# Optimization experiments

Hardware: AMD Instinct MI355X
Metric: run time of the kernel (lower is better)

The kernel has to match this reference:

```python
import jax, jax.numpy as jnp
import numpy as np

N = 20000          # num proposals (nodes)
E = 320000         # num edges
IN = 4096          # roi feature dim
EMB = 200          # glove embed dim
HID = 512          # hidden dim
NH = 8             # heads (conv1)
HC = HID // NH     # 64 per-head channels
NCLS = 151         # VG object classes
NEG_SLOPE = 0.2    # PyG GATConv leaky_relu slope


def setup_inputs() -> dict:
    key = jax.random.key(0)
    ks = jax.random.split(key, 18)
    d_in1 = IN + EMB + 128  # 4424, conv1 input dim
    inp = {
        "roi_features": jax.random.normal(ks[0], (N, IN), jnp.float32),
        "box_info": jax.random.uniform(ks[1], (N, 9), jnp.float32),
        # embedding tables
        "emb1": jax.random.normal(ks[2], (NCLS, EMB), jnp.float32) * 0.02,
        "emb2": jax.random.normal(ks[3], (NCLS, EMB), jnp.float32) * 0.02,
        # bbox MLP 9 -> 32 -> 128
        "bw1": jax.random.normal(ks[4], (9, 32), jnp.float32) / np.sqrt(9),
        "bb1": jnp.zeros((32,), jnp.float32),
        "bw2": jax.random.normal(ks[5], (32, 128), jnp.float32) / np.sqrt(32),
        "bb2": jnp.zeros((128,), jnp.float32),
        # GATConv1: d_in1 -> 8 heads x 64, concat
        "W1": jax.random.normal(ks[6], (d_in1, NH * HC), jnp.float32) / np.sqrt(d_in1),
        "a_src1": jax.random.normal(ks[7], (NH, HC), jnp.float32) * 0.1,
        "a_dst1": jax.random.normal(ks[8], (NH, HC), jnp.float32) * 0.1,
        "bias1": jnp.zeros((NH * HC,), jnp.float32),
        # GATConv2: 512 -> 512, 1 head, concat=False
        "W2": jax.random.normal(ks[9], (HID, HID), jnp.float32) / np.sqrt(HID),
        "a_src2": jax.random.normal(ks[10], (1, HID), jnp.float32) * 0.1,
        "a_dst2": jax.random.normal(ks[11], (1, HID), jnp.float32) * 0.1,
        "bias2": jnp.zeros((HID,), jnp.float32),
        # int inputs
        "obj_labels": jax.random.randint(ks[12], (N,), 0, NCLS, jnp.int32),
        "edge_index": jax.random.randint(ks[13], (2, E), 0, N, jnp.int32),
    }
    return inp


def _segment_softmax(logits, seg, n):
    # logits: [E, H]; softmax over edges sharing the same destination seg id
    m = jax.ops.segment_max(logits, seg, num_segments=n)
    e = jnp.exp(logits - m[seg])
    s = jax.ops.segment_sum(e, seg, num_segments=n)
    return e / (s[seg] + 1e-16)


def _gat_conv(x, src, dst, W, a_src, a_dst, bias, concat):
    # PyG GATConv (self-loops already included in src/dst); dropout off (eval)
    n = x.shape[0]
    H, C = a_src.shape
    h = (x @ W).reshape(n, H, C)                      # [N, H, C]
    al_s = jnp.einsum('nhc,hc->nh', h, a_src)         # [N, H]
    al_d = jnp.einsum('nhc,hc->nh', h, a_dst)
    logits = jax.nn.leaky_relu(al_s[src] + al_d[dst], NEG_SLOPE)  # [E, H]
    alpha = _segment_softmax(logits, dst, n)          # [E, H]
    out = jax.ops.segment_sum(alpha[:, :, None] * h[src], dst, num_segments=n)
    out = out.reshape(n, H * C) if concat else out.mean(axis=1)
    return out + bias


def reference(roi_features, box_info, emb1, emb2, bw1, bb1, bw2, bb2,
              W1, a_src1, a_dst1, bias1, W2, a_src2, a_dst2, bias2,
              obj_labels, edge_index):
    n = roi_features.shape[0]
    # predcls mode: GT labels -> embedding lookup
    obj_embed = emb1[obj_labels]                              # [N, 200]
    pos = jax.nn.relu(box_info @ bw1 + bb1)
    pos = jax.nn.relu(pos @ bw2 + bb2)                        # [N, 128]
    x = jnp.concatenate([roi_features, obj_embed, pos], -1)  # [N, 4424]

    # add self-loops (PyG GATConv default)
    ar = jnp.arange(n, dtype=edge_index.dtype)
    src = jnp.concatenate([edge_index[0], ar])
    dst = jnp.concatenate([edge_index[1], ar])

    edge_f1 = jax.nn.elu(_gat_conv(x, src, dst, W1, a_src1, a_dst1, bias1, True))
    obj_feats = _gat_conv(edge_f1, src, dst, W2, a_src2, a_dst2, bias2, False)

    obj_dists = jax.nn.one_hot(obj_labels, NCLS, dtype=jnp.float32)
    edge_pre_rep = jnp.concatenate([roi_features, obj_feats, emb2[obj_labels]], -1)
    return obj_dists, obj_labels, edge_pre_rep
```

## Files before the change

### kernel.cpp

```cpp
#include <hip/hip_runtime.h>
#include <hip/hip_bf16.h>

#define NNODES 20000
#define NEDGES 320000
#define ETOT   (NEDGES + NNODES)
#define KPADX  4224
#define SK     4
#define KC     (KPADX / SK)
#define MPAD   20096
#define NCLS   151
#define EPRW   4808
#define OUT_LAB_OFF  3020000L
#define OUT_EPR_OFF  3040000L
#define NSLOPE 0.2f

typedef __attribute__((ext_vector_type(8))) short bf16x8;
typedef __attribute__((ext_vector_type(4))) float f32x4;
typedef __attribute__((ext_vector_type(4))) short s16x4;

__device__ __forceinline__ short f2bf(float v) {
  union { __hip_bfloat16 b; short s; } u;
  u.b = __float2bfloat16(v);
  return u.s;
}

__device__ __forceinline__ float bf2f(short s) {
  union { float f; unsigned u; } x;
  x.u = ((unsigned)(unsigned short)s) << 16;
  return x.f;
}

__device__ __forceinline__ void gld16(const short* g, short* l) {
  __builtin_amdgcn_global_load_lds(
      (const __attribute__((address_space(1))) unsigned int*)g,
      (__attribute__((address_space(3))) unsigned int*)l, 16, 0, 0);
}

#define QB0 10000
#define QB1 (QB0 + 5000)
#define QB2 (QB1 + 1584)
#define QB3 (QB2 + 2112)
#define QB4 (QB3 + 256)
#define QB5 (QB4 + 1329)
#define QB6 (QB5 + 151)

__global__ __launch_bounds__(256) void mega_prep_kernel(
    const float* __restrict__ roi, const float* __restrict__ box,
    const float* __restrict__ emb1, const float* __restrict__ emb2,
    const float* __restrict__ bw1, const float* __restrict__ bb1,
    const float* __restrict__ bw2, const float* __restrict__ bb2,
    const float* __restrict__ W1, const float* __restrict__ W2,
    const int* __restrict__ labels, const int* __restrict__ ei,
    short* __restrict__ x, short* __restrict__ w1t, short* __restrict__ w2t,
    short* __restrict__ ef1, int* __restrict__ deg,
    float* __restrict__ als2, float* __restrict__ ald2,
    float* __restrict__ E1, float* __restrict__ dout) {
  const int b = blockIdx.x;
  const int tid = threadIdx.x;

  __shared__ float hids[4][32];
  __shared__ float tile[32][33];

  if (b < QB0) {
    const int base = b * 2048 + tid;
    f32x4 v[8];
#pragma unroll
    for (int k = 0; k < 8; ++k)
      v[k] = *(const f32x4*)&roi[(long)(base + k * 256) * 4];
#pragma unroll
    for (int k = 0; k < 8; ++k) {
      const int t = base + k * 256;
      const int node = t >> 10, cq = t & 1023;
      __builtin_nontemporal_store(v[k],
          (f32x4*)&dout[OUT_EPR_OFF + (long)node * EPRW + cq * 4]);
      s16x4 bb;
      bb.x = f2bf(v[k].x); bb.y = f2bf(v[k].y);
      bb.z = f2bf(v[k].z); bb.w = f2bf(v[k].w);
      *(s16x4*)&x[(long)node * KPADX + cq * 4] = bb;
    }
  } else if (b < QB1) {
    const int w = tid >> 6;
    const int lane = tid & 63;
    const int nd = (b - QB0) * 4 + w;
    if (lane < 32) {
      float a = bb1[lane];
#pragma unroll
      for (int i = 0; i < 9; ++i) a += box[nd * 9 + i] * bw1[i * 32 + lane];
      hids[w][lane] = a > 0.f ? a : 0.f;
    }
    __syncthreads();
    const long xrow = (long)nd * KPADX;
#pragma unroll
    for (int jj = 0; jj < 2; ++jj) {
      const int j = lane + jj * 64;
      float a = bb2[j];
#pragma unroll
      for (int i = 0; i < 32; ++i) a += hids[w][i] * bw2[i * 128 + j];
      a = a > 0.f ? a : 0.f;
      x[xrow + 4096 + j] = f2bf(a);
    }
    const int lab = labels[nd];
    float* epr = dout + OUT_EPR_OFF + (long)nd * EPRW;
    if (lane < 50) {
      const f32x4 e2 = *(const f32x4*)&emb2[lab * 200 + lane * 4];
      __builtin_nontemporal_store(e2, (f32x4*)&epr[4608 + lane * 4]);
    }
    for (int j = lane; j < NCLS; j += 64)
      dout[(long)nd * NCLS + j] = (j == lab) ? 1.f : 0.f;
    if (lane == 0) dout[OUT_LAB_OFF + nd] = (float)lab;
  } else if (b < QB2) {
    const int t = (b - QB1) * 256 + tid;
    if (t < 96 * KPADX) x[(long)NNODES * KPADX + t] = 0;
    if (t < 96 * 512)   ef1[(long)NNODES * 512 + t] = 0;
    if (t < MPAD)       { als2[t] = 0.f; ald2[t] = 0.f; }
  } else if (b < QB3) {
    const int t = b - QB2;
    const int n0 = (t % 16) * 32;
    const int k0 = (t / 16) * 32;
    const int tx = tid & 31, ty = tid >> 5;
#pragma unroll
    for (int i = ty; i < 32; i += 8) {
      const int kp = k0 + i;
      const int src = kp < 4096 ? kp : kp + 200;
      tile[i][tx] = W1[(long)src * 512 + (n0 + tx)];
    }
    __syncthreads();
#pragma unroll
    for (int i = ty; i < 32; i += 8)
      w1t[(long)(n0 + i) * KPADX + (k0 + tx)] = f2bf(tile[tx][i]);
  } else if (b < QB4) {
    const int t = b - QB3;
    const int n0 = (t % 16) * 32;
    const int k0 = (t / 16) * 32;
    const int tx = tid & 31, ty = tid >> 5;
#pragma unroll
    for (int i = ty; i < 32; i += 8)
      tile[i][tx] = W2[(long)(k0 + i) * 512 + (n0 + tx)];
    __syncthreads();
#pragma unroll
    for (int i = ty; i < 32; i += 8)
      w2t[(long)(n0 + i) * 512 + (k0 + tx)] = f2bf(tile[tx][i]);
  } else if (b < QB5) {
    const int e = (b - QB4) * 256 + tid;
    if (e < ETOT) {
      const int d = (e < NEDGES) ? ei[NEDGES + e] : (e - NEDGES);
      atomicAdd(&deg[d], 1);
    }
  } else {
    const int c = b - QB5;
#pragma unroll
    for (int jj = 0; jj < 2; ++jj) {
      const int j = tid + jj * 256;
      float a = 0.f;
      for (int k = 0; k < 200; ++k)
        a += emb1[c * 200 + k] * W1[(long)(4096 + k) * 512 + j];
      E1[c * 512 + j] = a;
    }
  }
}

__global__ __launch_bounds__(256) void scan_kernel(const int* __restrict__ deg,
                                                   int* __restrict__ off,
                                                   int* __restrict__ cur) {
  __shared__ int part[256];
  const int tid = threadIdx.x;
  const int chunk = (NNODES + 255) / 256;
  int start = tid * chunk;
  int end = start + chunk; if (end > NNODES) end = NNODES;
  int s = 0;
  for (int i = start; i < end; ++i) s += deg[i];
  part[tid] = s;
  __syncthreads();
  for (int d = 1; d < 256; d <<= 1) {
    const int v = (tid >= d) ? part[tid - d] : 0;
    __syncthreads();
    part[tid] += v;
    __syncthreads();
  }
  int base = part[tid] - s;
  for (int i = start; i < end; ++i) { off[i] = base; cur[i] = base; base += deg[i]; }
}

__global__ void csr_fill_kernel(const int* __restrict__ ei, int* __restrict__ cur,
                                int* __restrict__ csrs) {
  const int e = blockIdx.x * 256 + threadIdx.x;
  if (e >= ETOT) return;
  const int s = (e < NEDGES) ? ei[e] : (e - NEDGES);
  const int d = (e < NEDGES) ? ei[NEDGES + e] : (e - NEDGES);
  unsigned slot = (unsigned)atomicAdd(&cur[d], 1);
  if (slot >= ETOT) slot = 0;
  csrs[slot] = s;
}

__global__ __launch_bounds__(256) void gemm_split(const short* __restrict__ A,
                                                  const short* __restrict__ BT,
                                                  short* __restrict__ hp) {
  __shared__ short As[2][4096];
  __shared__ short Bs[2][4096];
  const int tid = threadIdx.x;
  const int lane = tid & 63;
  const int w = tid >> 6;
  const int wr = w >> 1, wc = w & 1;
  const int wid = (blockIdx.x & 7) * 314 + ((int)blockIdx.x >> 3);
  const long bm = (long)(wid >> 4) * 128;
  const int  sk = (wid >> 2) & 3;
  const long bn = (long)(wid & 3) * 128;

  f32x4 acc[4][4] = {};

  const int ksw = ((lane & 3) ^ ((lane >> 3) & 3)) * 8;
  const short* gA0 = A + (bm + w * 32 + (lane >> 2)) * (long)KPADX + sk * KC + ksw;
  const short* gA1 = gA0 + 16L * KPADX;
  const short* gB0 = BT + (bn + w * 32 + (lane >> 2)) * (long)KPADX + sk * KC + ksw;
  const short* gB1 = gB0 + 16L * KPADX;

  const int lofs = w * 1024;
  const int sw = ((lane >> 4) ^ (((lane & 15) >> 1) & 3)) * 8;
  const int ar = (wr * 64 + (lane & 15)) * 32 + sw;
  const int br = (wc * 64 + (lane & 15)) * 32 + sw;

  gld16(gA0, &As[0][lofs]); gld16(gA1, &As[0][lofs + 512]);
  gld16(gB0, &Bs[0][lofs]); gld16(gB1, &Bs[0][lofs + 512]);
  gA0 += 32; gA1 += 32; gB0 += 32; gB1 += 32;

  const int NT = KC / 32;
  int cur = 0;
  for (int t = 0; t < NT; ++t) {
    if (t + 1 < NT) {
      gld16(gA0, &As[cur ^ 1][lofs]); gld16(gA1, &As[cur ^ 1][lofs + 512]);
      gld16(gB0, &Bs[cur ^ 1][lofs]); gld16(gB1, &Bs[cur ^ 1][lofs + 512]);
      gA0 += 32; gA1 += 32; gB0 += 32; gB1 += 32;
      asm volatile("s_waitcnt vmcnt(4)" ::: "memory");
    } else {
      asm volatile("s_waitcnt vmcnt(0)" ::: "memory");
    }
    __builtin_amdgcn_s_barrier();
    bf16x8 a[4], b[4];
#pragma unroll
    for (int mi = 0; mi < 4; ++mi) a[mi] = *(const bf16x8*)&As[cur][ar + mi * 512];
#pragma unroll
    for (int ni = 0; ni < 4; ++ni) b[ni] = *(const bf16x8*)&Bs[cur][br + ni * 512];
#pragma unroll
    for (int mi = 0; mi < 4; ++mi)
#pragma unroll
      for (int ni = 0; ni < 4; ++ni)
        acc[mi][ni] = __builtin_amdgcn_mfma_f32_16x16x32_bf16(a[mi], b[ni], acc[mi][ni], 0, 0, 0);
    __builtin_amdgcn_s_barrier();
    cur ^= 1;
  }

  short* Cp = hp + (long)sk * MPAD * 512;
#pragma unroll
  for (int mi = 0; mi < 4; ++mi) {
#pragma unroll
    for (int ni = 0; ni < 4; ++ni) {
      const long row0 = bm + wr * 64 + mi * 16 + (lane >> 4) * 4;
      const long col  = bn + wc * 64 + ni * 16 + (lane & 15);
#pragma unroll
      for (int r = 0; r < 4; ++r)
        Cp[(row0 + r) * 512 + col] = f2bf(acc[mi][ni][r]);
    }
  }
}

__global__ __launch_bounds__(256) void reduce1_kernel(short* __restrict__ hp,
    const float* __restrict__ E1, const int* __restrict__ labels,
    const float* __restrict__ aS, const float* __restrict__ aD,
    float* __restrict__ als, float* __restrict__ ald) {
  const int row = blockIdx.x * 4 + (threadIdx.x >> 6);
  const int lane = threadIdx.x & 63;
  const int c0 = lane * 8;
  const long base = (long)row * 512 + c0;
  float v[8] = {};
#pragma unroll
  for (int s = 0; s < SK; ++s) {
    const bf16x8 p = *(const bf16x8*)&hp[(long)s * MPAD * 512 + base];
#pragma unroll
    for (int j = 0; j < 8; ++j) v[j] += bf2f(p[j]);
  }
  const int lab = (row < NNODES) ? labels[row] : 0;
  const float* e1r = E1 + (long)lab * 512;
#pragma unroll
  for (int j = 0; j < 8; ++j) v[j] += e1r[c0 + j];
  bf16x8 o;
#pragma unroll
  for (int j = 0; j < 8; ++j) o[j] = f2bf(v[j]);
  *(bf16x8*)&hp[base] = o;
  float s_ = 0.f, d_ = 0.f;
#pragma unroll
  for (int j = 0; j < 8; ++j) {
    s_ += v[j] * aS[c0 + j];
    d_ += v[j] * aD[c0 + j];
  }
#pragma unroll
  for (int oo = 1; oo < 8; oo <<= 1) {
    s_ += __shfl_xor(s_, oo);
    d_ += __shfl_xor(d_, oo);
  }
  if ((lane & 7) == 0) {
    const int head = lane >> 3;
    als[row * 8 + head] = s_;
    ald[row * 8 + head] = d_;
  }
}

__global__ __launch_bounds__(256) void gemm_bt(const short* __restrict__ A,
                                               const short* __restrict__ BT,
                                               short* __restrict__ C,
                                               const float* __restrict__ aS,
                                               const float* __restrict__ aD,
                                               float* __restrict__ als,
                                               float* __restrict__ ald,
                                               int Kpad, int Ncols, int H) {
  __shared__ short As[2][4096];
  __shared__ short Bs[2][4096];
  const int tid = threadIdx.x;
  const int lane = tid & 63;
  const int w = tid >> 6;
  const int wr = w >> 1, wc = w & 1;
  const int nbn = Ncols >> 7;
  const long bm = (long)((int)blockIdx.x / nbn) * 128;
  const long bn = (long)((int)blockIdx.x % nbn) * 128;

  f32x4 acc[4][4] = {};

  const int ksw = ((lane & 3) ^ ((lane >> 3) & 3)) * 8;
  const short* gA0 = A + (bm + w * 32 + (lane >> 2)) * (long)Kpad + ksw;
  const short* gA1 = gA0 + 16L * Kpad;
  const short* gB0 = BT + (bn + w * 32 + (lane >> 2)) * (long)Kpad + ksw;
  const short* gB1 = gB0 + 16L * Kpad;

  const int lofs = w * 1024;
  const int sw = ((lane >> 4) ^ (((lane & 15) >> 1) & 3)) * 8;
  const int ar = (wr * 64 + (lane & 15)) * 32 + sw;
  const int br = (wc * 64 + (lane & 15)) * 32 + sw;

  gld16(gA0, &As[0][lofs]); gld16(gA1, &As[0][lofs + 512]);
  gld16(gB0, &Bs[0][lofs]); gld16(gB1, &Bs[0][lofs + 512]);
  gA0 += 32; gA1 += 32; gB0 += 32; gB1 += 32;

  const int NT = Kpad / 32;
  int cur = 0;
  for (int t = 0; t < NT; ++t) {
    if (t + 1 < NT) {
      gld16(gA0, &As[cur ^ 1][lofs]); gld16(gA1, &As[cur ^ 1][lofs + 512]);
      gld16(gB0, &Bs[cur ^ 1][lofs]); gld16(gB1, &Bs[cur ^ 1][lofs + 512]);
      gA0 += 32; gA1 += 32; gB0 += 32; gB1 += 32;
      asm volatile("s_waitcnt vmcnt(4)" ::: "memory");
    } else {
      asm volatile("s_waitcnt vmcnt(0)" ::: "memory");
    }
    __builtin_amdgcn_s_barrier();
    bf16x8 a[4], b[4];
#pragma unroll
    for (int mi = 0; mi < 4; ++mi) a[mi] = *(const bf16x8*)&As[cur][ar + mi * 512];
#pragma unroll
    for (int ni = 0; ni < 4; ++ni) b[ni] = *(const bf16x8*)&Bs[cur][br + ni * 512];
#pragma unroll
    for (int mi = 0; mi < 4; ++mi)
#pragma unroll
      for (int ni = 0; ni < 4; ++ni)
        acc[mi][ni] = __builtin_amdgcn_mfma_f32_16x16x32_bf16(a[mi], b[ni], acc[mi][ni], 0, 0, 0);
    __builtin_amdgcn_s_barrier();
    cur ^= 1;
  }

  const int colb = (int)bn + wc * 64 + (lane & 15);

#pragma unroll
  for (int mi = 0; mi < 4; ++mi) {
#pragma unroll
    for (int ni = 0; ni < 4; ++ni) {
      const long row0 = bm + wr * 64 + mi * 16 + (lane >> 4) * 4;
      const long col  = bn + wc * 64 + ni * 16 + (lane & 15);
#pragma unroll
      for (int r = 0; r < 4; ++r)
        C[(row0 + r) * (long)Ncols + col] = f2bf(acc[mi][ni][r]);
    }
  }

  float asv[4], adv[4];
#pragma unroll
  for (int ni = 0; ni < 4; ++ni) {
    asv[ni] = aS[colb + ni * 16];
    adv[ni] = aD[colb + ni * 16];
  }
  const int head = (H == 8) ? (((int)bn >> 6) + wc) : 0;
#pragma unroll
  for (int mi = 0; mi < 4; ++mi) {
#pragma unroll
    for (int r = 0; r < 4; ++r) {
      float s = 0.f, d = 0.f;
#pragma unroll
      for (int ni = 0; ni < 4; ++ni) {
        const float v = acc[mi][ni][r];
        s += v * asv[ni];
        d += v * adv[ni];
      }
#pragma unroll
      for (int o = 1; o < 16; o <<= 1) {
        s += __shfl_xor(s, o);
        d += __shfl_xor(d, o);
      }
      if ((lane & 15) == 0) {
        const long row = bm + wr * 64 + mi * 16 + (lane >> 4) * 4 + r;
        atomicAdd(&als[row * H + head], s);
        atomicAdd(&ald[row * H + head], d);
      }
    }
  }
}

__global__ __launch_bounds__(256) void gather1_kernel(const int* __restrict__ off,
    const int* __restrict__ csrs,
    const float* __restrict__ als, const float* __restrict__ ald,
    const short* __restrict__ h1, const float* __restrict__ bias,
    short* __restrict__ ef1) {
  const int dn = blockIdx.x * 4 + (threadIdx.x >> 6);
  const int lane = threadIdx.x & 63;
  const int c0 = lane * 8;
  const int head = lane >> 3;
  const int beg = off[dn];
  const int end = (dn == NNODES - 1) ? ETOT : off[dn + 1];
  const float ad = ald[dn * 8 + head];
  float sum = 0.f;
  float acc[8] = {};
  for (int i = beg; i < end; ++i) {
    int s = csrs[i];
    if ((unsigned)s >= NNODES) s = 0;
    float l = als[s * 8 + head] + ad;
    l = l > 0.f ? l : NSLOPE * l;
    const float wgt = expf(l);
    sum += wgt;
    const bf16x8 hv = *(const bf16x8*)&h1[(long)s * 512 + c0];
#pragma unroll
    for (int j = 0; j < 8; ++j) acc[j] += wgt * bf2f(hv[j]);
  }
  const float inv = 1.f / (sum + 1e-16f);
  bf16x8 outv;
#pragma unroll
  for (int j = 0; j < 8; ++j) {
    float r = acc[j] * inv + bias[c0 + j];
    r = r > 0.f ? r : expm1f(r);
    outv[j] = f2bf(r);
  }
  *(bf16x8*)&ef1[(long)dn * 512 + c0] = outv;
}

__global__ __launch_bounds__(256) void gather2_kernel(const int* __restrict__ off,
    const int* __restrict__ csrs,
    const float* __restrict__ als, const float* __restrict__ ald,
    const short* __restrict__ h2, const float* __restrict__ bias,
    float* __restrict__ dout) {
  const int dn = blockIdx.x * 4 + (threadIdx.x >> 6);
  const int lane = threadIdx.x & 63;
  const int c0 = lane * 8;
  const int beg = off[dn];
  const int end = (dn == NNODES - 1) ? ETOT : off[dn + 1];
  const float ad = ald[dn];
  float sum = 0.f;
  float acc[8] = {};
  for (int i = beg; i < end; ++i) {
    int s = csrs[i];
    if ((unsigned)s >= NNODES) s = 0;
    float l = als[s] + ad;
    l = l > 0.f ? l : NSLOPE * l;
    const float wgt = expf(l);
    sum += wgt;
    const bf16x8 hv = *(const bf16x8*)&h2[(long)s * 512 + c0];
#pragma unroll
    for (int j = 0; j < 8; ++j) acc[j] += wgt * bf2f(hv[j]);
  }
  const float inv = 1.f / (sum + 1e-16f);
  float* epr = dout + OUT_EPR_OFF + (long)dn * EPRW + 4096;
  f32x4 o0, o1;
  o0.x = acc[0] * inv + bias[c0 + 0];
  o0.y = acc[1] * inv + bias[c0 + 1];
  o0.z = acc[2] * inv + bias[c0 + 2];
  o0.w = acc[3] * inv + bias[c0 + 3];
  o1.x = acc[4] * inv + bias[c0 + 4];
  o1.y = acc[5] * inv + bias[c0 + 5];
  o1.z = acc[6] * inv + bias[c0 + 6];
  o1.w = acc[7] * inv + bias[c0 + 7];
  __builtin_nontemporal_store(o0, (f32x4*)&epr[c0]);
  __builtin_nontemporal_store(o1, (f32x4*)&epr[c0 + 4]);
}

extern "C" void kernel_launch(void* const* d_in, const int* in_sizes, int n_in,
                              void* d_out, int out_size, void* d_ws, size_t ws_size,
                              hipStream_t stream) {
  const float* roi  = (const float*)d_in[0];
  const float* box  = (const float*)d_in[1];
  const float* emb1 = (const float*)d_in[2];
  const float* emb2 = (const float*)d_in[3];
  const float* bw1  = (const float*)d_in[4];
  const float* bb1  = (const float*)d_in[5];
  const float* bw2  = (const float*)d_in[6];
  const float* bb2  = (const float*)d_in[7];
  const float* W1   = (const float*)d_in[8];
  const float* as1  = (const float*)d_in[9];
  const float* ad1  = (const float*)d_in[10];
  const float* b1   = (const float*)d_in[11];
  const float* W2   = (const float*)d_in[12];
  const float* as2  = (const float*)d_in[13];
  const float* ad2  = (const float*)d_in[14];
  const float* b2   = (const float*)d_in[15];
  const int* labels = (const int*)d_in[16];
  const int* ei     = (const int*)d_in[17];
  float* dout = (float*)d_out;

  char* wsb = (char*)d_ws;
  size_t o = 0;
  auto alloc = [&](size_t bytes) -> void* {
    void* p = wsb + o;
    o += (bytes + 255) & ~(size_t)255;
    return p;
  };
  short* x    = (short*)alloc((size_t)MPAD * KPADX * 2);
  short* w1t  = (short*)alloc((size_t)512 * KPADX * 2);
  short* hp   = (short*)alloc((size_t)SK * MPAD * 512 * 2);
  short* h1   = hp;
  short* ef1  = (short*)alloc((size_t)MPAD * 512 * 2);
  short* w2t  = (short*)alloc((size_t)512 * 512 * 2);
  short* h2   = (short*)alloc((size_t)MPAD * 512 * 2);
  float* als1 = (float*)alloc((size_t)MPAD * 8 * 4);
  float* ald1 = (float*)alloc((size_t)MPAD * 8 * 4);
  float* als2 = (float*)alloc((size_t)MPAD * 4);
  float* ald2 = (float*)alloc((size_t)MPAD * 4);
  float* E1   = (float*)alloc((size_t)NCLS * 512 * 4);
  int*   deg  = (int*)alloc((size_t)NNODES * 4);
  int*   offs = (int*)alloc((size_t)NNODES * 4);
  int*   cur  = (int*)alloc((size_t)NNODES * 4);
  int*   csrs = (int*)alloc((size_t)ETOT * 4);

  const int EB = (ETOT + 255) / 256;

  hipMemsetAsync(deg, 0, (size_t)NNODES * 4, stream);

  hipLaunchKernelGGL(mega_prep_kernel, dim3(QB6), dim3(256), 0, stream,
                     roi, box, emb1, emb2, bw1, bb1, bw2, bb2, W1, W2,
                     labels, ei, x, w1t, w2t, ef1, deg,
                     als2, ald2, E1, dout);
  hipLaunchKernelGGL(scan_kernel, dim3(1), dim3(256), 0, stream, deg, offs, cur);
  hipLaunchKernelGGL(csr_fill_kernel, dim3(EB), dim3(256), 0, stream, ei, cur, csrs);
  hipLaunchKernelGGL(gemm_split, dim3(157 * SK * 4), dim3(256), 0, stream,
                     x, w1t, hp);
  hipLaunchKernelGGL(reduce1_kernel, dim3(MPAD / 4), dim3(256), 0, stream,
                     hp, E1, labels, as1, ad1, als1, ald1);
  hipLaunchKernelGGL(gather1_kernel, dim3(NNODES / 4), dim3(256), 0, stream,
                     offs, csrs, als1, ald1, h1, b1, ef1);
  hipLaunchKernelGGL(gemm_bt, dim3(157 * 4), dim3(256), 0, stream,
                     ef1, w2t, h2, as2, ad2, als2, ald2, 512, 512, 1);
  hipLaunchKernelGGL(gather2_kernel, dim3(NNODES / 4), dim3(256), 0, stream,
                     offs, csrs, als2, ald2, h2, b2, dout);
}
```

Measured before the change: 577.6 us.

## Fold CSR fill into split-K GEMM launch, halve split-K, drop LDS swizzle

Merges the CSR fill kernel into the first GEMM launch as extra trailing blocks, removing one kernel launch and letting edge scatter overlap with the GEMM. Split-K drops from 4 to 2, which halves the partial-sum buffer traffic in the reduce step but gives fewer, longer GEMM blocks. The XOR swizzle on shared-memory tile addresses is removed in both GEMMs, which simplifies addressing but may bring back LDS bank conflicts. Since hp is still sized for SK partials and reduce1 reads hp, the reduce step must agree with the new SK.

```diff
diff --git a/kernel.cpp b/kernel.cpp
--- a/kernel.cpp
+++ b/kernel.cpp
@@ -5,8 +5,10 @@
 #define NEDGES 320000
 #define ETOT   (NEDGES + NNODES)
 #define KPADX  4224
-#define SK     4
+#define SK     2
 #define KC     (KPADX / SK)
+#define NGEMM1 (157 * SK * 4)
+#define EB     ((ETOT + 255) / 256)
 #define MPAD   20096
 #define NCLS   151
 #define EPRW   4808
@@ -181,43 +183,44 @@
   for (int i = start; i < end; ++i) { off[i] = base; cur[i] = base; base += deg[i]; }
 }
 
-__global__ void csr_fill_kernel(const int* __restrict__ ei, int* __restrict__ cur,
-                                int* __restrict__ csrs) {
-  const int e = blockIdx.x * 256 + threadIdx.x;
-  if (e >= ETOT) return;
-  const int s = (e < NEDGES) ? ei[e] : (e - NEDGES);
-  const int d = (e < NEDGES) ? ei[NEDGES + e] : (e - NEDGES);
-  unsigned slot = (unsigned)atomicAdd(&cur[d], 1);
-  if (slot >= ETOT) slot = 0;
-  csrs[slot] = s;
-}
-
 __global__ __launch_bounds__(256) void gemm_split(const short* __restrict__ A,
                                                   const short* __restrict__ BT,
-                                                  short* __restrict__ hp) {
+                                                  short* __restrict__ hp,
+                                                  const int* __restrict__ ei,
+                                                  int* __restrict__ cur_,
+                                                  int* __restrict__ csrs) {
+  const int tid = threadIdx.x;
+  if ((int)blockIdx.x >= NGEMM1) {
+    const int e = ((int)blockIdx.x - NGEMM1) * 256 + tid;
+    if (e < ETOT) {
+      const int s = (e < NEDGES) ? ei[e] : (e - NEDGES);
+      const int d = (e < NEDGES) ? ei[NEDGES + e] : (e - NEDGES);
+      unsigned slot = (unsigned)atomicAdd(&cur_[d], 1);
+      if (slot >= ETOT) slot = 0;
+      csrs[slot] = s;
+    }
+    return;
+  }
   __shared__ short As[2][4096];
   __shared__ short Bs[2][4096];
-  const int tid = threadIdx.x;
   const int lane = tid & 63;
   const int w = tid >> 6;
   const int wr = w >> 1, wc = w & 1;
-  const int wid = (blockIdx.x & 7) * 314 + ((int)blockIdx.x >> 3);
-  const long bm = (long)(wid >> 4) * 128;
-  const int  sk = (wid >> 2) & 3;
+  const int wid = (blockIdx.x & 7) * 157 + ((int)blockIdx.x >> 3);
+  const long bm = (long)(wid >> 3) * 128;
+  const int  sk = (wid >> 2) & 1;
   const long bn = (long)(wid & 3) * 128;
 
   f32x4 acc[4][4] = {};
 
-  const int ksw = ((lane & 3) ^ ((lane >> 3) & 3)) * 8;
-  const short* gA0 = A + (bm + w * 32 + (lane >> 2)) * (long)KPADX + sk * KC + ksw;
+  const short* gA0 = A + (bm + w * 32 + (lane >> 2)) * (long)KPADX + sk * KC + (lane & 3) * 8;
   const short* gA1 = gA0 + 16L * KPADX;
-  const short* gB0 = BT + (bn + w * 32 + (lane >> 2)) * (long)KPADX + sk * KC + ksw;
+  const short* gB0 = BT + (bn + w * 32 + (lane >> 2)) * (long)KPADX + sk * KC + (lane & 3) * 8;
   const short* gB1 = gB0 + 16L * KPADX;
 
   const int lofs = w * 1024;
-  const int sw = ((lane >> 4) ^ (((lane & 15) >> 1) & 3)) * 8;
-  const int ar = (wr * 64 + (lane & 15)) * 32 + sw;
-  const int br = (wc * 64 + (lane & 15)) * 32 + sw;
+  const int ar = (wr * 64 + (lane & 15)) * 32 + (lane >> 4) * 8;
+  const int br = (wc * 64 + (lane & 15)) * 32 + (lane >> 4) * 8;
 
   gld16(gA0, &As[0][lofs]); gld16(gA1, &As[0][lofs + 512]);
   gld16(gB0, &Bs[0][lofs]); gld16(gB1, &Bs[0][lofs + 512]);
@@ -324,16 +327,14 @@
 
   f32x4 acc[4][4] = {};
 
-  const int ksw = ((lane & 3) ^ ((lane >> 3) & 3)) * 8;
-  const short* gA0 = A + (bm + w * 32 + (lane >> 2)) * (long)Kpad + ksw;
+  const short* gA0 = A + (bm + w * 32 + (lane >> 2)) * (long)Kpad + (lane & 3) * 8;
   const short* gA1 = gA0 + 16L * Kpad;
-  const short* gB0 = BT + (bn + w * 32 + (lane >> 2)) * (long)Kpad + ksw;
+  const short* gB0 = BT + (bn + w * 32 + (lane >> 2)) * (long)Kpad + (lane & 3) * 8;
   const short* gB1 = gB0 + 16L * Kpad;
 
   const int lofs = w * 1024;
-  const int sw = ((lane >> 4) ^ (((lane & 15) >> 1) & 3)) * 8;
-  const int ar = (wr * 64 + (lane & 15)) * 32 + sw;
-  const int br = (wc * 64 + (lane & 15)) * 32 + sw;
+  const int ar = (wr * 64 + (lane & 15)) * 32 + (lane >> 4) * 8;
+  const int br = (wc * 64 + (lane & 15)) * 32 + (lane >> 4) * 8;
 
   gld16(gA0, &As[0][lofs]); gld16(gA1, &As[0][lofs + 512]);
   gld16(gB0, &Bs[0][lofs]); gld16(gB1, &Bs[0][lofs + 512]);
@@ -533,8 +534,6 @@
   int*   cur  = (int*)alloc((size_t)NNODES * 4);
   int*   csrs = (int*)alloc((size_t)ETOT * 4);
 
-  const int EB = (ETOT + 255) / 256;
-
   hipMemsetAsync(deg, 0, (size_t)NNODES * 4, stream);
 
   hipLaunchKernelGGL(mega_prep_kernel, dim3(QB6), dim3(256), 0, stream,
@@ -542,9 +541,8 @@
                      labels, ei, x, w1t, w2t, ef1, deg,
                      als2, ald2, E1, dout);
   hipLaunchKernelGGL(scan_kernel, dim3(1), dim3(256), 0, stream, deg, offs, cur);
-  hipLaunchKernelGGL(csr_fill_kernel, dim3(EB), dim3(256), 0, stream, ei, cur, csrs);
-  hipLaunchKernelGGL(gemm_split, dim3(157 * SK * 4), dim3(256), 0, stream,
-                     x, w1t, hp);
+  hipLaunchKernelGGL(gemm_split, dim3(NGEMM1 + EB), dim3(256), 0, stream,
+                     x, w1t, hp, ei, cur, csrs);
   hipLaunchKernelGGL(reduce1_kernel, dim3(MPAD / 4), dim3(256), 0, stream,
                      hp, E1, labels, as1, ad1, als1, ald1);
   hipLaunchKernelGGL(gather1_kernel, dim3(NNODES / 4), dim3(256), 0, stream,
```

Result: faster. 546.6 us (-5.4%).
